# Optimization experiments

Hardware: AMD Instinct MI355X
Metric: run time of the kernel (lower is better)

Reference implementation:

```python
import jax, jax.numpy as jnp
import numpy as np

B, N = 1, 1024
C_A, C_Z, H = 768, 128, 16
CH = C_A // H  # 48
INV_SQRT_CH = float(1.0 / np.sqrt(CH))


def _ln(x, w, b):
    # torch.nn.LayerNorm over last dim, eps=1e-5
    m = jnp.mean(x, axis=-1, keepdims=True)
    v = jnp.mean(jnp.square(x - m), axis=-1, keepdims=True)
    return (x - m) * jax.lax.rsqrt(v + 1e-5) * w + b


def setup_inputs() -> dict:
    key = jax.random.key(0)
    ks = jax.random.split(key, 8)
    rn = lambda k, shape, sc: jax.random.normal(k, shape, dtype=jnp.float32) * sc
    return {
        "a": rn(ks[0], (B, N, C_A), 1.0),
        "z": rn(ks[1], (B, N, N, C_Z), 1.0),
        "mask": jnp.ones((B, N), dtype=jnp.float32),
        "ln_a_w": jnp.ones((C_A,), jnp.float32),
        "ln_a_b": jnp.zeros((C_A,), jnp.float32),
        "ln_z_w": jnp.ones((C_Z,), jnp.float32),
        "ln_z_b": jnp.zeros((C_Z,), jnp.float32),
        "Wq": rn(ks[2], (C_A, H * CH), 0.02),
        "bq": jnp.zeros((H * CH,), jnp.float32),
        "Wk": rn(ks[3], (C_A, H * CH), 0.02),
        "Wv": rn(ks[4], (C_A, H * CH), 0.02),
        "Wb": rn(ks[5], (C_Z, H), 0.02),
        "Wg": rn(ks[6], (C_A, H * CH), 0.02),
        "Wo": rn(ks[7], (H * CH, C_A), 0.02),
    }


def reference(a, z, mask, ln_a_w, ln_a_b, ln_z_w, ln_z_b, Wq, bq, Wk, Wv, Wb, Wg, Wo):
    an = _ln(a, ln_a_w, ln_a_b)                                  # [B, N, C_A]
    q = (an @ Wq + bq).reshape(B, N, H, CH)
    k = (an @ Wk).reshape(B, N, H, CH)
    v = (an @ Wv).reshape(B, N, H, CH)
    # pair bias: LayerNorm(z) -> per-head scalar bias [B, N, N, H]
    bpair = _ln(z, ln_z_w, ln_z_b) @ Wb
    mbias = (mask - 1.0)[:, None, None, :] * 1e9                  # [B, 1, 1, N]
    logits = jnp.einsum('bqhc,bkhc->bhqk', q, k) * INV_SQRT_CH
    logits = logits + jnp.transpose(bpair, (0, 3, 1, 2)) + mbias  # [B, H, N, N]
    attn = jax.nn.softmax(logits, axis=-1)
    o = jnp.einsum('bhqk,bkhc->bqhc', attn, v)                    # [B, N, H, CH]
    g = jax.nn.sigmoid(an @ Wg).reshape(B, N, H, CH)
    out = (g * o).reshape(B, N, H * CH) @ Wo                      # [B, N, C_A]
    return out
```

## Files before the change

kernel.cpp:

```cpp
#include <hip/hip_runtime.h>

#define NSEQ 1024
#define CA   768
#define CZ   128
#define NH   16
#define CHD  48
#define HC   768
#define INV_SQRT_CH 0.14433756729740643f

typedef float v4f __attribute__((ext_vector_type(4)));
typedef short v8s __attribute__((ext_vector_type(8)));

__device__ __forceinline__ short f2bf(float f) {
  union { float f; unsigned u; } v; v.f = f;
  unsigned r = v.u + 0x7fffu + ((v.u >> 16) & 1u);
  return (short)(r >> 16);
}
__device__ __forceinline__ float bf2f(short s) {
  union { unsigned u; float f; } v;
  v.u = ((unsigned)(unsigned short)s) << 16;
  return v.f;
}
__device__ __forceinline__ unsigned cvtpk(float lo, float hi) {
  unsigned r;
  asm("v_cvt_pk_bf16_f32 %0, %1, %2" : "=v"(r) : "v"(lo), "v"(hi));
  return r;
}

__global__ __launch_bounds__(256) void k_front(
    const float* __restrict__ lnzw, const float* __restrict__ lnzb,
    const float* __restrict__ Wb, short* __restrict__ wWp, float* __restrict__ S1bW,
    const float* __restrict__ Wq, const float* __restrict__ Wk,
    const float* __restrict__ Wv, const float* __restrict__ Wg,
    const float* __restrict__ Wo, short* __restrict__ WT, short* __restrict__ WoT,
    const float* __restrict__ a, const float* __restrict__ lnaw,
    const float* __restrict__ lnab, short* __restrict__ anb)
{
  __shared__ __align__(16) char fsm[64 * 65 * 4];
  const int bid = blockIdx.x;
  const int t = threadIdx.x;

  if (bid == 0) {
    const int s = t >> 6, l = t & 63;
    const int r16 = l & 15, cg = l >> 4;
    float v[8];
    #pragma unroll
    for (int j = 0; j < 8; ++j) {
      int d = s * 32 + cg * 8 + j;
      v[j] = lnzw[d] * Wb[d * NH + r16];
    }
    uint4 pk;
    pk.x = cvtpk(v[0], v[1]); pk.y = cvtpk(v[2], v[3]);
    pk.z = cvtpk(v[4], v[5]); pk.w = cvtpk(v[6], v[7]);
    *(uint4*)(wWp + (s * 64 + l) * 8) = pk;
    if (t < NH) {
      float s1 = 0.f, bw = 0.f;
      for (int d = 0; d < CZ; ++d) {
        float wb = Wb[d * NH + t];
        s1 += bf2f(f2bf(lnzw[d] * wb));
        bw += lnzb[d] * wb;
      }
      S1bW[t] = s1;
      S1bW[NH + t] = bw;
    }
  } else if (bid <= 720) {
    float (*tile)[65] = (float(*)[65])fsm;
    const int cb = bid - 1;
    const int mat = cb / 144, rem = cb % 144;
    const int tk = rem % 12, tn = rem / 12;
    const int k0 = tk * 64, n0 = tn * 64;
    const float* __restrict__ W =
        (mat == 0) ? Wq : (mat == 1) ? Wk : (mat == 2) ? Wv : (mat == 3) ? Wg : Wo;
    const float s = (mat == 0) ? INV_SQRT_CH : 1.f;
    const int rr = t >> 4, cc = (t & 15) * 4;
    #pragma unroll
    for (int r = 0; r < 4; ++r) {
      v4f v = *(const v4f*)(W + (size_t)(k0 + r * 16 + rr) * HC + n0 + cc);
      tile[r * 16 + rr][cc + 0] = v[0];
      tile[r * 16 + rr][cc + 1] = v[1];
      tile[r * 16 + rr][cc + 2] = v[2];
      tile[r * 16 + rr][cc + 3] = v[3];
    }
    __syncthreads();
    short* dst = (mat < 4) ? (WT + (size_t)mat * HC * CA) : WoT;
    #pragma unroll
    for (int r = 0; r < 4; ++r) {
      const int nr = r * 16 + rr;
      uint2 pk;
      pk.x = cvtpk(tile[cc + 0][nr] * s, tile[cc + 1][nr] * s);
      pk.y = cvtpk(tile[cc + 2][nr] * s, tile[cc + 3][nr] * s);
      *(uint2*)(dst + (size_t)(n0 + nr) * CA + k0 + cc) = pk;
    }
  } else {
    float* red = (float*)fsm;
    const int row = bid - 721;
    const float* ar = a + (size_t)row * CA;
    float x[3];
    float s = 0.f, s2 = 0.f;
    #pragma unroll
    for (int i = 0; i < 3; ++i) {
      x[i] = ar[t + i * 256];
      s += x[i]; s2 += x[i] * x[i];
    }
    #pragma unroll
    for (int off = 1; off < 64; off <<= 1) {
      s += __shfl_xor(s, off);
      s2 += __shfl_xor(s2, off);
    }
    const int wv = t >> 6;
    if ((t & 63) == 0) { red[wv] = s; red[4 + wv] = s2; }
    __syncthreads();
    s = red[0] + red[1] + red[2] + red[3];
    s2 = red[4] + red[5] + red[6] + red[7];
    const float m = s * (1.f / CA);
    const float var = s2 * (1.f / CA) - m * m;
    const float rs = rsqrtf(var + 1e-5f);
    #pragma unroll
    for (int i = 0; i < 3; ++i) {
      int c = t + i * 256;
      anb[(size_t)row * CA + c] = f2bf((x[i] - m) * rs * lnaw[c] + lnab[c]);
    }
  }
}

__global__ __launch_bounds__(256) void k2_gemm(
    const short* __restrict__ anb, const short* __restrict__ WT,
    const float* __restrict__ bq,
    short* __restrict__ qb, short* __restrict__ kb, short* __restrict__ vT,
    float* __restrict__ gbuf)
{
  __shared__ __align__(16) short As[128 * 40];
  __shared__ __align__(16) short Bs[128 * 40];
  const int tid = threadIdx.x;
  const int w = tid >> 6, l = tid & 63;
  const int r16 = l & 15, cg = l >> 4;
  const int bm = blockIdx.x & 7;
  const int bnb = blockIdx.x >> 3;
  const int m0 = bm * 128, n0 = bnb * 128;
  const int wr = w >> 1, wc = w & 1;
  const int strow = w * 16 + (l >> 2);
  const int scol = (l & 3) * 8;

  v4f acc[4][4];
  #pragma unroll
  for (int i = 0; i < 4; ++i)
    #pragma unroll
    for (int j = 0; j < 4; ++j)
      acc[i][j] = (v4f){0.f, 0.f, 0.f, 0.f};

  for (int k0 = 0; k0 < CA; k0 += 32) {
    v8s av0 = *(const v8s*)(anb + (size_t)(m0 + strow) * CA + k0 + scol);
    v8s av1 = *(const v8s*)(anb + (size_t)(m0 + 64 + strow) * CA + k0 + scol);
    v8s bv0 = *(const v8s*)(WT + (size_t)(n0 + strow) * CA + k0 + scol);
    v8s bv1 = *(const v8s*)(WT + (size_t)(n0 + 64 + strow) * CA + k0 + scol);
    __syncthreads();
    *(v8s*)(As + (size_t)strow * 40 + scol) = av0;
    *(v8s*)(As + (size_t)(64 + strow) * 40 + scol) = av1;
    *(v8s*)(Bs + (size_t)strow * 40 + scol) = bv0;
    *(v8s*)(Bs + (size_t)(64 + strow) * 40 + scol) = bv1;
    __syncthreads();
    v8s a[4], b[4];
    #pragma unroll
    for (int m = 0; m < 4; ++m)
      a[m] = *(const v8s*)(As + (wr * 64 + m * 16 + r16) * 40 + cg * 8);
    #pragma unroll
    for (int n = 0; n < 4; ++n)
      b[n] = *(const v8s*)(Bs + (wc * 64 + n * 16 + r16) * 40 + cg * 8);
    #pragma unroll
    for (int m = 0; m < 4; ++m)
      #pragma unroll
      for (int n = 0; n < 4; ++n)
        acc[m][n] = __builtin_amdgcn_mfma_f32_16x16x32_bf16(a[m], b[n], acc[m][n], 0, 0, 0);
  }

  const int matsel = n0 / HC;
  #pragma unroll
  for (int n = 0; n < 4; ++n) {
    const int nc = (n0 % HC) + wc * 64 + n * 16 + r16;
    const int rbase = m0 + wr * 64 + cg * 4;
    if (matsel == 0) {
      const float bqs = bq[nc] * INV_SQRT_CH;
      #pragma unroll
      for (int m = 0; m < 4; ++m)
        #pragma unroll
        for (int j = 0; j < 4; ++j)
          qb[(size_t)(rbase + m * 16 + j) * HC + nc] = f2bf(acc[m][n][j] + bqs);
    } else if (matsel == 1) {
      #pragma unroll
      for (int m = 0; m < 4; ++m)
        #pragma unroll
        for (int j = 0; j < 4; ++j)
          kb[(size_t)(rbase + m * 16 + j) * HC + nc] = f2bf(acc[m][n][j]);
    } else if (matsel == 2) {
      #pragma unroll
      for (int m = 0; m < 4; ++m) {
        uint2 pk;
        pk.x = cvtpk(acc[m][n][0], acc[m][n][1]);
        pk.y = cvtpk(acc[m][n][2], acc[m][n][3]);
        *(uint2*)(vT + (size_t)nc * NSEQ + rbase + m * 16) = pk;
      }
    } else {
      #pragma unroll
      for (int m = 0; m < 4; ++m)
        #pragma unroll
        for (int j = 0; j < 4; ++j)
          gbuf[(size_t)(rbase + m * 16 + j) * HC + nc] =
              1.f / (1.f + __expf(-acc[m][n][j]));
    }
  }
}

#define BL_SH 68
__global__ __launch_bounds__(256) void k3_z(
    const float* __restrict__ z, const short* __restrict__ wWp,
    const float* __restrict__ S1bW, short* __restrict__ bpair)
{
  __shared__ __align__(16) short blds[4][16 * BL_SH];
  const int tid = threadIdx.x;
  const int w = tid >> 6, l = tid & 63;
  const int r16 = l & 15, cg = l >> 4;
  const int q = blockIdx.x >> 2;
  const int kw = ((blockIdx.x & 3) << 8) + w * 64;
  short* bl = &blds[w][0];

  v8s bfrag[4];
  #pragma unroll
  for (int s = 0; s < 4; ++s) bfrag[s] = *(const v8s*)(wWp + (s * 64 + l) * 8);
  const float S1 = S1bW[r16];
  const float bW = S1bW[NH + r16];

  const float* __restrict__ zbase = z + ((size_t)q * NSEQ + kw + r16) * CZ;

  v4f zb[8];
  #pragma unroll
  for (int s = 0; s < 4; ++s) {
    zb[2 * s]     = *(const v4f*)(zbase + s * 32 + cg * 8);
    zb[2 * s + 1] = *(const v4f*)(zbase + s * 32 + cg * 8 + 4);
  }

  for (int kt = 0; kt < 4; ++kt) {
    v4f zn[8];
    if (kt < 3) {
      const float* __restrict__ zr2 = zbase + (size_t)(kt + 1) * 16 * CZ;
      #pragma unroll
      for (int s = 0; s < 4; ++s) {
        zn[2 * s]     = *(const v4f*)(zr2 + s * 32 + cg * 8);
        zn[2 * s + 1] = *(const v4f*)(zr2 + s * 32 + cg * 8 + 4);
      }
    }

    float sum = 0.f, sum2 = 0.f;
    v8s afrag[4];
    #pragma unroll
    for (int s = 0; s < 4; ++s) {
      v4f z0 = zb[2 * s], z1 = zb[2 * s + 1];
      #pragma unroll
      for (int j = 0; j < 4; ++j) {
        sum += z0[j] + z1[j];
        sum2 += z0[j] * z0[j] + z1[j] * z1[j];
      }
      union { v8s s8; unsigned u[4]; } fu;
      fu.u[0] = cvtpk(z0[0], z0[1]);
      fu.u[1] = cvtpk(z0[2], z0[3]);
      fu.u[2] = cvtpk(z1[0], z1[1]);
      fu.u[3] = cvtpk(z1[2], z1[3]);
      afrag[s] = fu.s8;
    }
    sum  += __shfl_xor(sum, 16);  sum  += __shfl_xor(sum, 32);
    sum2 += __shfl_xor(sum2, 16); sum2 += __shfl_xor(sum2, 32);
    const float mean = sum * (1.f / CZ);
    const float var = sum2 * (1.f / CZ) - mean * mean;
    const float rs = rsqrtf(var + 1e-5f);

    v4f acc = {0.f, 0.f, 0.f, 0.f};
    #pragma unroll
    for (int s = 0; s < 4; ++s)
      acc = __builtin_amdgcn_mfma_f32_16x16x32_bf16(afrag[s], bfrag[s], acc, 0, 0, 0);

    float bv[4];
    #pragma unroll
    for (int j = 0; j < 4; ++j) {
      int src = cg * 4 + j;
      float mj = __shfl(mean, src);
      float rj = __shfl(rs, src);
      bv[j] = rj * (acc[j] - mj * S1) + bW;
    }
    *(unsigned*)&bl[r16 * BL_SH + kt * 16 + cg * 4]     = cvtpk(bv[0], bv[1]);
    *(unsigned*)&bl[r16 * BL_SH + kt * 16 + cg * 4 + 2] = cvtpk(bv[2], bv[3]);

    if (kt < 3) {
      #pragma unroll
      for (int i = 0; i < 8; ++i) zb[i] = zn[i];
    }
  }

  asm volatile("s_waitcnt lgkmcnt(0)" ::: "memory");
  __builtin_amdgcn_sched_barrier(0);

  const int h = l >> 2, ck = (l & 3) * 16;
  v8s o0 = *(const v8s*)(bl + h * BL_SH + ck);
  v8s o1 = *(const v8s*)(bl + h * BL_SH + ck + 8);
  short* dst = bpair + (size_t)h * NSEQ * NSEQ + (size_t)q * NSEQ + kw + ck;
  *(v8s*)(dst)     = o0;
  *(v8s*)(dst + 8) = o1;
}

#define PL_STRIDE 136
#define PO_STRIDE 52
__global__ __launch_bounds__(512) void k45_attn(
    const short* __restrict__ qb, const short* __restrict__ kb,
    const short* __restrict__ vT, const short* __restrict__ bpair,
    const float* __restrict__ mask, const float* __restrict__ gbuf,
    short* __restrict__ gob)
{
  const int h = blockIdx.x & 15;
  const int qt = blockIdx.x >> 4;
  const int tid = threadIdx.x;
  const int w = tid >> 6, l = tid & 63;
  const int r16 = l & 15, cg = l >> 4;
  const int q0 = qt * 16;
  const int k0 = w * 128;

  __shared__ __align__(16) short plds[8][16 * PL_STRIDE];
  __shared__ __align__(16) float po_lds[8][16][PO_STRIDE];
  __shared__ __align__(16) float ml_lds[8][16][2];
  short* pl = &plds[w][0];

  const v8s vzero = {0, 0, 0, 0, 0, 0, 0, 0};
  v8s qf0, qf1;
  {
    const short* qp = qb + (size_t)(q0 + r16) * HC + h * CHD;
    qf0 = *(const v8s*)(qp + cg * 8);
    qf1 = (cg < 2) ? *(const v8s*)(qp + 32 + cg * 8) : vzero;
  }

  const size_t bpb = (size_t)h * NSEQ * NSEQ;
  {
    const int srow = l >> 2;
    const int scol = (l & 3) * 32;
    const short* bsrc = bpair + bpb + (size_t)(q0 + srow) * NSEQ + k0 + scol;
    short* bdst = pl + srow * PL_STRIDE + scol;
    v8s t0 = *(const v8s*)(bsrc);
    v8s t1 = *(const v8s*)(bsrc + 8);
    v8s t2 = *(const v8s*)(bsrc + 16);
    v8s t3 = *(const v8s*)(bsrc + 24);
    *(v8s*)(bdst)      = t0;
    *(v8s*)(bdst + 8)  = t1;
    *(v8s*)(bdst + 16) = t2;
    *(v8s*)(bdst + 24) = t3;
  }

  v4f cs[8];
  #pragma unroll
  for (int kt = 0; kt < 8; ++kt) {
    const short* kp = kb + (size_t)(k0 + kt * 16 + r16) * HC + h * CHD;
    v8s b0 = *(const v8s*)(kp + cg * 8);
    v8s b1 = (cg < 2) ? *(const v8s*)(kp + 32 + cg * 8) : vzero;
    v4f tacc = {0.f, 0.f, 0.f, 0.f};
    tacc = __builtin_amdgcn_mfma_f32_16x16x32_bf16(qf0, b0, tacc, 0, 0, 0);
    tacc = __builtin_amdgcn_mfma_f32_16x16x32_bf16(qf1, b1, tacc, 0, 0, 0);
    cs[kt] = tacc;
  }

  #pragma unroll
  for (int kt = 0; kt < 8; ++kt) {
    const int kc = k0 + kt * 16 + r16;
    const float mb = (mask[kc] - 1.f) * 1e9f;
    #pragma unroll
    for (int j = 0; j < 4; ++j)
      cs[kt][j] += bf2f(pl[(cg * 4 + j) * PL_STRIDE + kt * 16 + r16]) + mb;
  }

  float mx4[4], ls4[4];
  #pragma unroll
  for (int j = 0; j < 4; ++j) {
    float mx = fmaxf(fmaxf(fmaxf(cs[0][j], cs[1][j]), fmaxf(cs[2][j], cs[3][j])),
                     fmaxf(fmaxf(cs[4][j], cs[5][j]), fmaxf(cs[6][j], cs[7][j])));
    mx = fmaxf(mx, __shfl_xor(mx, 1));
    mx = fmaxf(mx, __shfl_xor(mx, 2));
    mx = fmaxf(mx, __shfl_xor(mx, 4));
    mx = fmaxf(mx, __shfl_xor(mx, 8));
    mx4[j] = mx;
    float p[8];
    #pragma unroll
    for (int kt = 0; kt < 8; ++kt) p[kt] = __expf(cs[kt][j] - mx);
    float rsum = ((p[0] + p[1]) + (p[2] + p[3])) + ((p[4] + p[5]) + (p[6] + p[7]));
    rsum += __shfl_xor(rsum, 1);
    rsum += __shfl_xor(rsum, 2);
    rsum += __shfl_xor(rsum, 4);
    rsum += __shfl_xor(rsum, 8);
    ls4[j] = rsum;
    const int rowb = (cg * 4 + j) * PL_STRIDE;
    #pragma unroll
    for (int t2 = 0; t2 < 4; ++t2) {
      unsigned u = cvtpk(p[2 * t2], p[2 * t2 + 1]);
      pl[rowb + (2 * t2) * 16 + r16] = (short)u;
      pl[rowb + (2 * t2 + 1) * 16 + r16] = (short)(u >> 16);
    }
  }
  asm volatile("s_waitcnt lgkmcnt(0)" ::: "memory");
  __builtin_amdgcn_sched_barrier(0);

  v4f of0 = {0, 0, 0, 0}, of1 = {0, 0, 0, 0}, of2 = {0, 0, 0, 0};
  #pragma unroll
  for (int ks4 = 0; ks4 < 4; ++ks4) {
    v8s pa = *(const v8s*)(pl + r16 * PL_STRIDE + ks4 * 32 + cg * 8);
    const short* vp = vT + (size_t)(h * CHD + r16) * NSEQ + k0 + ks4 * 32 + cg * 8;
    v8s bv0 = *(const v8s*)vp;
    v8s bv1 = *(const v8s*)(vp + 16 * NSEQ);
    v8s bv2 = *(const v8s*)(vp + 32 * NSEQ);
    of0 = __builtin_amdgcn_mfma_f32_16x16x32_bf16(pa, bv0, of0, 0, 0, 0);
    of1 = __builtin_amdgcn_mfma_f32_16x16x32_bf16(pa, bv1, of1, 0, 0, 0);
    of2 = __builtin_amdgcn_mfma_f32_16x16x32_bf16(pa, bv2, of2, 0, 0, 0);
  }

  #pragma unroll
  for (int j = 0; j < 4; ++j) {
    const int row = cg * 4 + j;
    po_lds[w][row][r16]      = of0[j];
    po_lds[w][row][16 + r16] = of1[j];
    po_lds[w][row][32 + r16] = of2[j];
    if (r16 == 0) {
      ml_lds[w][row][0] = mx4[j];
      ml_lds[w][row][1] = ls4[j];
    }
  }
  __syncthreads();

  {
    const int g = tid >> 5;
    const int lane = tid & 31;
    float mi[8], li[8];
    #pragma unroll
    for (int i = 0; i < 8; ++i) {
      mi[i] = ml_lds[i][g][0];
      li[i] = ml_lds[i][g][1];
    }
    float mstar = -1e30f;
    #pragma unroll
    for (int i = 0; i < 8; ++i) mstar = fmaxf(mstar, mi[i]);
    float wgt[8], L = 0.f;
    #pragma unroll
    for (int i = 0; i < 8; ++i) { wgt[i] = __expf(mi[i] - mstar); L += li[i] * wgt[i]; }
    const float inv = 1.f / L;
    const int q = q0 + g;
    {
      float o = 0.f;
      #pragma unroll
      for (int i = 0; i < 8; ++i) o += po_lds[i][g][lane] * wgt[i];
      const float gv = gbuf[(size_t)q * HC + h * CHD + lane];
      gob[(size_t)q * HC + h * CHD + lane] = f2bf(o * inv * gv);
    }
    if (lane < 16) {
      const int d = 32 + lane;
      float o = 0.f;
      #pragma unroll
      for (int i = 0; i < 8; ++i) o += po_lds[i][g][d] * wgt[i];
      const float gv = gbuf[(size_t)q * HC + h * CHD + d];
      gob[(size_t)q * HC + h * CHD + d] = f2bf(o * inv * gv);
    }
  }
}

__global__ __launch_bounds__(256) void k5_out(
    const short* __restrict__ gob, const short* __restrict__ WoT,
    float* __restrict__ out)
{
  __shared__ __align__(16) short As[64 * 40];
  __shared__ __align__(16) short Bs[64 * 40];
  const int tid = threadIdx.x;
  const int w = tid >> 6, l = tid & 63;
  const int r16 = l & 15, cg = l >> 4;
  const int bm = blockIdx.x & 15;
  const int bn = blockIdx.x >> 4;
  const int m0 = bm * 64, n0 = bn * 64;
  const int wr = w >> 1, wc = w & 1;
  const int strow = tid >> 2;
  const int scol = (tid & 3) * 8;

  v4f acc[2][2];
  #pragma unroll
  for (int i = 0; i < 2; ++i)
    #pragma unroll
    for (int j = 0; j < 2; ++j)
      acc[i][j] = (v4f){0.f, 0.f, 0.f, 0.f};

  for (int k0 = 0; k0 < CA; k0 += 32) {
    v8s av = *(const v8s*)(gob + (size_t)(m0 + strow) * CA + k0 + scol);
    v8s bv = *(const v8s*)(WoT + (size_t)(n0 + strow) * CA + k0 + scol);
    __syncthreads();
    *(v8s*)(As + (size_t)strow * 40 + scol) = av;
    *(v8s*)(Bs + (size_t)strow * 40 + scol) = bv;
    __syncthreads();
    v8s a[2], b[2];
    #pragma unroll
    for (int m = 0; m < 2; ++m)
      a[m] = *(const v8s*)(As + (wr * 32 + m * 16 + r16) * 40 + cg * 8);
    #pragma unroll
    for (int n = 0; n < 2; ++n)
      b[n] = *(const v8s*)(Bs + (wc * 32 + n * 16 + r16) * 40 + cg * 8);
    #pragma unroll
    for (int m = 0; m < 2; ++m)
      #pragma unroll
      for (int n = 0; n < 2; ++n)
        acc[m][n] = __builtin_amdgcn_mfma_f32_16x16x32_bf16(a[m], b[n], acc[m][n], 0, 0, 0);
  }

  #pragma unroll
  for (int n = 0; n < 2; ++n) {
    const int nc = n0 + wc * 32 + n * 16 + r16;
    const int rbase = m0 + wr * 32 + cg * 4;
    #pragma unroll
    for (int m = 0; m < 2; ++m)
      #pragma unroll
      for (int j = 0; j < 4; ++j)
        out[(size_t)(rbase + m * 16 + j) * CA + nc] = acc[m][n][j];
  }
}

extern "C" void kernel_launch(void* const* d_in, const int* in_sizes, int n_in,
                              void* d_out, int out_size, void* d_ws, size_t ws_size,
                              hipStream_t stream) {
  const float* a      = (const float*)d_in[0];
  const float* z      = (const float*)d_in[1];
  const float* mask   = (const float*)d_in[2];
  const float* ln_a_w = (const float*)d_in[3];
  const float* ln_a_b = (const float*)d_in[4];
  const float* ln_z_w = (const float*)d_in[5];
  const float* ln_z_b = (const float*)d_in[6];
  const float* Wq     = (const float*)d_in[7];
  const float* bq     = (const float*)d_in[8];
  const float* Wk     = (const float*)d_in[9];
  const float* Wv     = (const float*)d_in[10];
  const float* Wb     = (const float*)d_in[11];
  const float* Wg     = (const float*)d_in[12];
  const float* Wo     = (const float*)d_in[13];
  float* out = (float*)d_out;

  char* ws = (char*)d_ws;
  short* anb   = (short*)(ws);
  short* WT    = (short*)(ws + (2ull << 20));
  short* WoT   = (short*)(ws + (7ull << 20));
  short* qb    = (short*)(ws + (9ull << 20));
  short* kb    = (short*)(ws + (11ull << 20));
  short* vT    = (short*)(ws + (13ull << 20));
  float* gbuf  = (float*)(ws + (15ull << 20));
  short* wWp   = (short*)(ws + (19ull << 20));
  float* S1bW  = (float*)(ws + (19ull << 20) + 4096ull);
  short* gob   = (short*)(ws + (20ull << 20));
  short* bpair = (short*)(ws + (22ull << 20));

  k_front<<<1745, 256, 0, stream>>>(ln_z_w, ln_z_b, Wb, wWp, S1bW,
                                    Wq, Wk, Wv, Wg, Wo, WT, WoT,
                                    a, ln_a_w, ln_a_b, anb);
  k2_gemm<<<192, 256, 0, stream>>>(anb, WT, bq, qb, kb, vT, gbuf);
  k3_z<<<4096, 256, 0, stream>>>(z, wWp, S1bW, bpair);
  k45_attn<<<1024, 512, 0, stream>>>(qb, kb, vT, bpair, mask, gbuf, gob);
  k5_out<<<192, 256, 0, stream>>>(gob, WoT, out);
}
```

Baseline: 194.7 us.

## Merge QKVG GEMM and pair-bias kernels into one launch

Combines the projection GEMM kernel and the z layernorm/pair-bias kernel into one launch, with block index choosing which branch runs. The two stages are independent, so the small 192-block GEMM can overlap with the memory-bound z pass, and one launch and its tail are removed. The cost is a shared-memory footprint sized for the larger branch and register pressure set by the worse of the two branches, which may lower occupancy for the z blocks.

```diff
diff --git a/kernel.cpp b/kernel.cpp
--- a/kernel.cpp
+++ b/kernel.cpp
@@ -123,186 +123,182 @@
   }
 }
 
-__global__ __launch_bounds__(256) void k2_gemm(
+__global__ __launch_bounds__(256) void k23_mega(
     const short* __restrict__ anb, const short* __restrict__ WT,
-    const float* __restrict__ bq,
+    const float* __restrict__ bq, const float* __restrict__ z,
+    const short* __restrict__ wWp, const float* __restrict__ S1bW,
     short* __restrict__ qb, short* __restrict__ kb, short* __restrict__ vT,
-    float* __restrict__ gbuf)
+    float* __restrict__ gbuf, short* __restrict__ bpair)
 {
-  __shared__ __align__(16) short As[128 * 40];
-  __shared__ __align__(16) short Bs[128 * 40];
+  __shared__ __align__(16) char smem[20480];
   const int tid = threadIdx.x;
   const int w = tid >> 6, l = tid & 63;
   const int r16 = l & 15, cg = l >> 4;
-  const int bm = blockIdx.x & 7;
-  const int bnb = blockIdx.x >> 3;
-  const int m0 = bm * 128, n0 = bnb * 128;
-  const int wr = w >> 1, wc = w & 1;
-  const int strow = w * 16 + (l >> 2);
-  const int scol = (l & 3) * 8;
-
-  v4f acc[4][4];
-  #pragma unroll
-  for (int i = 0; i < 4; ++i)
-    #pragma unroll
-    for (int j = 0; j < 4; ++j)
-      acc[i][j] = (v4f){0.f, 0.f, 0.f, 0.f};
-
-  for (int k0 = 0; k0 < CA; k0 += 32) {
-    v8s av0 = *(const v8s*)(anb + (size_t)(m0 + strow) * CA + k0 + scol);
-    v8s av1 = *(const v8s*)(anb + (size_t)(m0 + 64 + strow) * CA + k0 + scol);
-    v8s bv0 = *(const v8s*)(WT + (size_t)(n0 + strow) * CA + k0 + scol);
-    v8s bv1 = *(const v8s*)(WT + (size_t)(n0 + 64 + strow) * CA + k0 + scol);
-    __syncthreads();
-    *(v8s*)(As + (size_t)strow * 40 + scol) = av0;
-    *(v8s*)(As + (size_t)(64 + strow) * 40 + scol) = av1;
-    *(v8s*)(Bs + (size_t)strow * 40 + scol) = bv0;
-    *(v8s*)(Bs + (size_t)(64 + strow) * 40 + scol) = bv1;
-    __syncthreads();
-    v8s a[4], b[4];
-    #pragma unroll
-    for (int m = 0; m < 4; ++m)
-      a[m] = *(const v8s*)(As + (wr * 64 + m * 16 + r16) * 40 + cg * 8);
-    #pragma unroll
-    for (int n = 0; n < 4; ++n)
-      b[n] = *(const v8s*)(Bs + (wc * 64 + n * 16 + r16) * 40 + cg * 8);
-    #pragma unroll
-    for (int m = 0; m < 4; ++m)
+
+  if (blockIdx.x < 192) {
+    short* As = (short*)smem;
+    short* Bs = (short*)(smem + 10240);
+    const int bm = blockIdx.x & 7;
+    const int bnb = blockIdx.x >> 3;
+    const int m0 = bm * 128, n0 = bnb * 128;
+    const int wr = w >> 1, wc = w & 1;
+    const int strow = w * 16 + (l >> 2);
+    const int scol = (l & 3) * 8;
+
+    v4f acc[4][4];
+    #pragma unroll
+    for (int i = 0; i < 4; ++i)
+      #pragma unroll
+      for (int j = 0; j < 4; ++j)
+        acc[i][j] = (v4f){0.f, 0.f, 0.f, 0.f};
+
+    for (int k0 = 0; k0 < CA; k0 += 32) {
+      v8s av0 = *(const v8s*)(anb + (size_t)(m0 + strow) * CA + k0 + scol);
+      v8s av1 = *(const v8s*)(anb + (size_t)(m0 + 64 + strow) * CA + k0 + scol);
+      v8s bv0 = *(const v8s*)(WT + (size_t)(n0 + strow) * CA + k0 + scol);
+      v8s bv1 = *(const v8s*)(WT + (size_t)(n0 + 64 + strow) * CA + k0 + scol);
+      __syncthreads();
+      *(v8s*)(As + (size_t)strow * 40 + scol) = av0;
+      *(v8s*)(As + (size_t)(64 + strow) * 40 + scol) = av1;
+      *(v8s*)(Bs + (size_t)strow * 40 + scol) = bv0;
+      *(v8s*)(Bs + (size_t)(64 + strow) * 40 + scol) = bv1;
+      __syncthreads();
+      v8s a[4], b[4];
+      #pragma unroll
+      for (int m = 0; m < 4; ++m)
+        a[m] = *(const v8s*)(As + (wr * 64 + m * 16 + r16) * 40 + cg * 8);
       #pragma unroll
       for (int n = 0; n < 4; ++n)
-        acc[m][n] = __builtin_amdgcn_mfma_f32_16x16x32_bf16(a[m], b[n], acc[m][n], 0, 0, 0);
-  }
-
-  const int matsel = n0 / HC;
-  #pragma unroll
-  for (int n = 0; n < 4; ++n) {
-    const int nc = (n0 % HC) + wc * 64 + n * 16 + r16;
-    const int rbase = m0 + wr * 64 + cg * 4;
-    if (matsel == 0) {
-      const float bqs = bq[nc] * INV_SQRT_CH;
+        b[n] = *(const v8s*)(Bs + (wc * 64 + n * 16 + r16) * 40 + cg * 8);
       #pragma unroll
       for (int m = 0; m < 4; ++m)
         #pragma unroll
-        for (int j = 0; j < 4; ++j)
-          qb[(size_t)(rbase + m * 16 + j) * HC + nc] = f2bf(acc[m][n][j] + bqs);
-    } else if (matsel == 1) {
-      #pragma unroll
-      for (int m = 0; m < 4; ++m)
-        #pragma unroll
-        for (int j = 0; j < 4; ++j)
-          kb[(size_t)(rbase + m * 16 + j) * HC + nc] = f2bf(acc[m][n][j]);
-    } else if (matsel == 2) {
-      #pragma unroll
-      for (int m = 0; m < 4; ++m) {
-        uint2 pk;
-        pk.x = cvtpk(acc[m][n][0], acc[m][n][1]);
-        pk.y = cvtpk(acc[m][n][2], acc[m][n][3]);
-        *(uint2*)(vT + (size_t)nc * NSEQ + rbase + m * 16) = pk;
+        for (int n = 0; n < 4; ++n)
+          acc[m][n] = __builtin_amdgcn_mfma_f32_16x16x32_bf16(a[m], b[n], acc[m][n], 0, 0, 0);
+    }
+
+    const int matsel = n0 / HC;
+    #pragma unroll
+    for (int n = 0; n < 4; ++n) {
+      const int nc = (n0 % HC) + wc * 64 + n * 16 + r16;
+      const int rbase = m0 + wr * 64 + cg * 4;
+      if (matsel == 0) {
+        const float bqs = bq[nc] * INV_SQRT_CH;
+        #pragma unroll
+        for (int m = 0; m < 4; ++m)
+          #pragma unroll
+          for (int j = 0; j < 4; ++j)
+            qb[(size_t)(rbase + m * 16 + j) * HC + nc] = f2bf(acc[m][n][j] + bqs);
+      } else if (matsel == 1) {
+        #pragma unroll
+        for (int m = 0; m < 4; ++m)
+          #pragma unroll
+          for (int j = 0; j < 4; ++j)
+            kb[(size_t)(rbase + m * 16 + j) * HC + nc] = f2bf(acc[m][n][j]);
+      } else if (matsel == 2) {
+        #pragma unroll
+        for (int m = 0; m < 4; ++m) {
+          uint2 pk;
+          pk.x = cvtpk(acc[m][n][0], acc[m][n][1]);
+          pk.y = cvtpk(acc[m][n][2], acc[m][n][3]);
+          *(uint2*)(vT + (size_t)nc * NSEQ + rbase + m * 16) = pk;
+        }
+      } else {
+        #pragma unroll
+        for (int m = 0; m < 4; ++m)
+          #pragma unroll
+          for (int j = 0; j < 4; ++j)
+            gbuf[(size_t)(rbase + m * 16 + j) * HC + nc] =
+                1.f / (1.f + __expf(-acc[m][n][j]));
       }
-    } else {
-      #pragma unroll
-      for (int m = 0; m < 4; ++m)
-        #pragma unroll
-        for (int j = 0; j < 4; ++j)
-          gbuf[(size_t)(rbase + m * 16 + j) * HC + nc] =
-              1.f / (1.f + __expf(-acc[m][n][j]));
-    }
-  }
-}
-
-#define BL_SH 68
-__global__ __launch_bounds__(256) void k3_z(
-    const float* __restrict__ z, const short* __restrict__ wWp,
-    const float* __restrict__ S1bW, short* __restrict__ bpair)
-{
-  __shared__ __align__(16) short blds[4][16 * BL_SH];
-  const int tid = threadIdx.x;
-  const int w = tid >> 6, l = tid & 63;
-  const int r16 = l & 15, cg = l >> 4;
-  const int q = blockIdx.x >> 2;
-  const int kw = ((blockIdx.x & 3) << 8) + w * 64;
-  short* bl = &blds[w][0];
-
-  v8s bfrag[4];
-  #pragma unroll
-  for (int s = 0; s < 4; ++s) bfrag[s] = *(const v8s*)(wWp + (s * 64 + l) * 8);
-  const float S1 = S1bW[r16];
-  const float bW = S1bW[NH + r16];
-
-  const float* __restrict__ zbase = z + ((size_t)q * NSEQ + kw + r16) * CZ;
-
-  v4f zb[8];
-  #pragma unroll
-  for (int s = 0; s < 4; ++s) {
-    zb[2 * s]     = *(const v4f*)(zbase + s * 32 + cg * 8);
-    zb[2 * s + 1] = *(const v4f*)(zbase + s * 32 + cg * 8 + 4);
-  }
-
-  for (int kt = 0; kt < 4; ++kt) {
-    v4f zn[8];
-    if (kt < 3) {
-      const float* __restrict__ zr2 = zbase + (size_t)(kt + 1) * 16 * CZ;
+    }
+  } else {
+    const int zbid = blockIdx.x - 192;
+    short* bl = (short*)smem + w * (16 * 68);
+    const int q = zbid >> 2;
+    const int kw = ((zbid & 3) << 8) + w * 64;
+
+    v8s bfrag[4];
+    #pragma unroll
+    for (int s = 0; s < 4; ++s) bfrag[s] = *(const v8s*)(wWp + (s * 64 + l) * 8);
+    const float S1 = S1bW[r16];
+    const float bW = S1bW[NH + r16];
+
+    const float* __restrict__ zbase = z + ((size_t)q * NSEQ + kw + r16) * CZ;
+
+    v4f zb[8];
+    #pragma unroll
+    for (int s = 0; s < 4; ++s) {
+      zb[2 * s]     = *(const v4f*)(zbase + s * 32 + cg * 8);
+      zb[2 * s + 1] = *(const v4f*)(zbase + s * 32 + cg * 8 + 4);
+    }
+
+    for (int kt = 0; kt < 4; ++kt) {
+      v4f zn[8];
+      if (kt < 3) {
+        const float* __restrict__ zr2 = zbase + (size_t)(kt + 1) * 16 * CZ;
+        #pragma unroll
+        for (int s = 0; s < 4; ++s) {
+          zn[2 * s]     = *(const v4f*)(zr2 + s * 32 + cg * 8);
+          zn[2 * s + 1] = *(const v4f*)(zr2 + s * 32 + cg * 8 + 4);
+        }
+      }
+
+      float sum = 0.f, sum2 = 0.f;
+      v8s afrag[4];
       #pragma unroll
       for (int s = 0; s < 4; ++s) {
-        zn[2 * s]     = *(const v4f*)(zr2 + s * 32 + cg * 8);
-        zn[2 * s + 1] = *(const v4f*)(zr2 + s * 32 + cg * 8 + 4);
+        v4f z0 = zb[2 * s], z1 = zb[2 * s + 1];
+        #pragma unroll
+        for (int j = 0; j < 4; ++j) {
+          sum += z0[j] + z1[j];
+          sum2 += z0[j] * z0[j] + z1[j] * z1[j];
+        }
+        union { v8s s8; unsigned u[4]; } fu;
+        fu.u[0] = cvtpk(z0[0], z0[1]);
+        fu.u[1] = cvtpk(z0[2], z0[3]);
+        fu.u[2] = cvtpk(z1[0], z1[1]);
+        fu.u[3] = cvtpk(z1[2], z1[3]);
+        afrag[s] = fu.s8;
       }
-    }
-
-    float sum = 0.f, sum2 = 0.f;
-    v8s afrag[4];
-    #pragma unroll
-    for (int s = 0; s < 4; ++s) {
-      v4f z0 = zb[2 * s], z1 = zb[2 * s + 1];
+      sum  += __shfl_xor(sum, 16);  sum  += __shfl_xor(sum, 32);
+      sum2 += __shfl_xor(sum2, 16); sum2 += __shfl_xor(sum2, 32);
+      const float mean = sum * (1.f / CZ);
+      const float var = sum2 * (1.f / CZ) - mean * mean;
+      const float rs = rsqrtf(var + 1e-5f);
+
+      v4f acc = {0.f, 0.f, 0.f, 0.f};
+      #pragma unroll
+      for (int s = 0; s < 4; ++s)
+        acc = __builtin_amdgcn_mfma_f32_16x16x32_bf16(afrag[s], bfrag[s], acc, 0, 0, 0);
+
+      float bv[4];
       #pragma unroll
       for (int j = 0; j < 4; ++j) {
-        sum += z0[j] + z1[j];
-        sum2 += z0[j] * z0[j] + z1[j] * z1[j];
+        int src = cg * 4 + j;
+        float mj = __shfl(mean, src);
+        float rj = __shfl(rs, src);
+        bv[j] = rj * (acc[j] - mj * S1) + bW;
       }
-      union { v8s s8; unsigned u[4]; } fu;
-      fu.u[0] = cvtpk(z0[0], z0[1]);
-      fu.u[1] = cvtpk(z0[2], z0[3]);
-      fu.u[2] = cvtpk(z1[0], z1[1]);
-      fu.u[3] = cvtpk(z1[2], z1[3]);
-      afrag[s] = fu.s8;
-    }
-    sum  += __shfl_xor(sum, 16);  sum  += __shfl_xor(sum, 32);
-    sum2 += __shfl_xor(sum2, 16); sum2 += __shfl_xor(sum2, 32);
-    const float mean = sum * (1.f / CZ);
-    const float var = sum2 * (1.f / CZ) - mean * mean;
-    const float rs = rsqrtf(var + 1e-5f);
-
-    v4f acc = {0.f, 0.f, 0.f, 0.f};
-    #pragma unroll
-    for (int s = 0; s < 4; ++s)
-      acc = __builtin_amdgcn_mfma_f32_16x16x32_bf16(afrag[s], bfrag[s], acc, 0, 0, 0);
-
-    float bv[4];
-    #pragma unroll
-    for (int j = 0; j < 4; ++j) {
-      int src = cg * 4 + j;
-      float mj = __shfl(mean, src);
-      float rj = __shfl(rs, src);
-      bv[j] = rj * (acc[j] - mj * S1) + bW;
-    }
-    *(unsigned*)&bl[r16 * BL_SH + kt * 16 + cg * 4]     = cvtpk(bv[0], bv[1]);
-    *(unsigned*)&bl[r16 * BL_SH + kt * 16 + cg * 4 + 2] = cvtpk(bv[2], bv[3]);
-
-    if (kt < 3) {
-      #pragma unroll
-      for (int i = 0; i < 8; ++i) zb[i] = zn[i];
-    }
-  }
-
-  asm volatile("s_waitcnt lgkmcnt(0)" ::: "memory");
-  __builtin_amdgcn_sched_barrier(0);
-
-  const int h = l >> 2, ck = (l & 3) * 16;
-  v8s o0 = *(const v8s*)(bl + h * BL_SH + ck);
-  v8s o1 = *(const v8s*)(bl + h * BL_SH + ck + 8);
-  short* dst = bpair + (size_t)h * NSEQ * NSEQ + (size_t)q * NSEQ + kw + ck;
-  *(v8s*)(dst)     = o0;
-  *(v8s*)(dst + 8) = o1;
+      *(unsigned*)&bl[r16 * 68 + kt * 16 + cg * 4]     = cvtpk(bv[0], bv[1]);
+      *(unsigned*)&bl[r16 * 68 + kt * 16 + cg * 4 + 2] = cvtpk(bv[2], bv[3]);
+
+      if (kt < 3) {
+        #pragma unroll
+        for (int i = 0; i < 8; ++i) zb[i] = zn[i];
+      }
+    }
+
+    asm volatile("s_waitcnt lgkmcnt(0)" ::: "memory");
+    __builtin_amdgcn_sched_barrier(0);
+
+    const int h = l >> 2, ck = (l & 3) * 16;
+    v8s o0 = *(const v8s*)(bl + h * 68 + ck);
+    v8s o1 = *(const v8s*)(bl + h * 68 + ck + 8);
+    short* dst = bpair + (size_t)h * NSEQ * NSEQ + (size_t)q * NSEQ + kw + ck;
+    *(v8s*)(dst)     = o0;
+    *(v8s*)(dst + 8) = o1;
+  }
 }
 
 #define PL_STRIDE 136
@@ -553,8 +549,8 @@
   k_front<<<1745, 256, 0, stream>>>(ln_z_w, ln_z_b, Wb, wWp, S1bW,
                                     Wq, Wk, Wv, Wg, Wo, WT, WoT,
                                     a, ln_a_w, ln_a_b, anb);
-  k2_gemm<<<192, 256, 0, stream>>>(anb, WT, bq, qb, kb, vT, gbuf);
-  k3_z<<<4096, 256, 0, stream>>>(z, wWp, S1bW, bpair);
+  k23_mega<<<192 + 4096, 256, 0, stream>>>(anb, WT, bq, z, wWp, S1bW,
+                                           qb, kb, vT, gbuf, bpair);
   k45_attn<<<1024, 512, 0, stream>>>(qb, kb, vT, bpair, mask, gbuf, gob);
   k5_out<<<192, 256, 0, stream>>>(gob, WoT, out);
 }
```

After: 173.1 us (median of 2 runs). 11.1% less time.
